# Kernel tuning notes

Hardware: AMD Instinct MI355X
Metric: run time of the kernel (lower is better)

Reference implementation:

```python
import jax, jax.numpy as jnp
import numpy as np

HEADS = 8
HIDDEN = 512
SEQ = 1024
BATCH = 8
SCALE = 1.2
TOPK = round(0.05 * SEQ)  # 51, as in mode='stocastic'


def setup_inputs() -> dict:
    key = jax.random.key(0)
    ks = jax.random.split(key, 12)
    d = HIDDEN
    s = 0.02
    return {
        "Query_x": jax.random.normal(ks[0], (BATCH, SEQ, d), jnp.float32),
        "KeyandValue_x": jax.random.normal(ks[1], (BATCH, SEQ, d), jnp.float32),
        "Wq": jax.random.normal(ks[2], (d, d), jnp.float32) * s,
        "bq": jnp.zeros((d,), jnp.float32),
        "Wk": jax.random.normal(ks[3], (d, d), jnp.float32) * s,
        "bk": jnp.zeros((d,), jnp.float32),
        "Wv": jax.random.normal(ks[4], (d, d), jnp.float32) * s,
        "bv": jnp.zeros((d,), jnp.float32),
        "Wo": jax.random.normal(ks[5], (d, d), jnp.float32) * s,
        "bo": jnp.zeros((d,), jnp.float32),
        "randidx": jax.random.randint(ks[6], (round(0.1 * SEQ),), 0, SEQ, jnp.int32),
    }


def _split_heads(x, B, S):
    # torch: split last dim into heads chunks, cat along dim 0 -> [heads*B, S, dk]
    dk = HIDDEN // HEADS
    return x.reshape(B, S, HEADS, dk).transpose(2, 0, 1, 3).reshape(HEADS * B, S, dk)


def _merge_heads(x, B, S):
    dk = HIDDEN // HEADS
    return x.reshape(HEADS, B, S, dk).transpose(1, 2, 0, 3).reshape(B, S, HIDDEN)


def moderate_attention(a, randidx):
    # a: [N, S, L] softmaxed attention. Scale top-k + random columns by SCALE,
    # then renormalize rows. torch scatter_ writes a*SCALE gathered from the
    # pre-scatter tensor, so duplicate indices are idempotent -> boolean mask.
    N, S, L = a.shape
    _, idx = jax.lax.top_k(a, TOPK)                       # [N, S, k]
    rand_b = jnp.broadcast_to(randidx.astype(idx.dtype), (N, S, randidx.shape[0]))
    all_idx = jnp.concatenate([idx, rand_b], axis=-1)      # [N, S, k+r]
    n_ix = jnp.arange(N)[:, None, None]
    q_ix = jnp.arange(S)[None, :, None]
    sel = jnp.zeros(a.shape, bool).at[n_ix, q_ix, all_idx].set(True)
    a2 = jnp.where(sel, a * SCALE, a)
    return a2 / jnp.sum(a2, axis=-1, keepdims=True)


def reference(Query_x, KeyandValue_x, Wq, bq, Wk, bk, Wv, bv, Wo, bo, randidx):
    B, S, _ = Query_x.shape
    dk = HIDDEN // HEADS
    Q = _split_heads(Query_x @ Wq + bq, B, S)          # [H*B, S, dk]
    K = _split_heads(KeyandValue_x @ Wk + bk, B, S)
    V = _split_heads(KeyandValue_x @ Wv + bv, B, S)
    scores = jnp.einsum('nqd,nkd->nqk', Q, K) / jnp.sqrt(jnp.float32(dk))
    a = jax.nn.softmax(scores, axis=-1)
    a = moderate_attention(a, randidx)
    out = jnp.einsum('nqk,nkd->nqd', a, V)
    return _merge_heads(out, B, S) @ Wo + bo
```

## Files before the change

### kernel.cpp

```cpp
#include <hip/hip_runtime.h>
#include <stdint.h>

typedef unsigned short ushort_t;
typedef __bf16 bf16x8 __attribute__((ext_vector_type(8)));
typedef _Float16 f16x8v __attribute__((ext_vector_type(8)));
typedef __fp16 fp16x2 __attribute__((ext_vector_type(2)));
typedef float f32x4 __attribute__((ext_vector_type(4)));

#define SEQ   1024
#define DK    64
#define TOPK_N 51
#define RSCALE 1.2f
#define LOG2E    1.44269504089f
#define LOG2_12  0.26303440583f

#define OFF_WT  0
#define OFF_Q   (4*512*512)
#define OFF_K   (OFF_Q  + 64*1024*64)
#define OFF_V   (OFF_K  + 64*1024*64)
#define OFF_A   (OFF_V  + 64*1024*64)
#define OFF_MASK (OFF_A + 8192*512)

static __device__ __forceinline__ ushort_t f2bf(float f){
  union { float f; unsigned u; } x; x.f = f;
  unsigned r = x.u + 0x7FFFu + ((x.u >> 16) & 1u);
  return (ushort_t)(r >> 16);
}
static __device__ __forceinline__ ushort_t f2h(float f){
  union { _Float16 h; ushort_t u; } x; x.h = (_Float16)f; return x.u;
}
static __device__ __forceinline__ float h2f(ushort_t u){
  union { ushort_t u; _Float16 h; } x; x.u = u; return (float)x.h;
}
static __device__ __forceinline__ unsigned pk2(float a, float b){
  union { fp16x2 h; unsigned u; } x;
  x.h = __builtin_amdgcn_cvt_pkrtz(a, b);
  return x.u;
}
static __device__ __forceinline__ unsigned pkrne(float a, float b){
  return (unsigned)f2h(a) | ((unsigned)f2h(b) << 16);
}
static __device__ __forceinline__ bf16x8 frag16(const ushort_t* p){
  union { uint4 u; bf16x8 b; } x; x.u = *(const uint4*)p; return x.b;
}
static __device__ __forceinline__ f16x8v frag16h(const ushort_t* p){
  union { uint4 u; f16x8v h; } x; x.u = *(const uint4*)p; return x.h;
}
static __device__ __forceinline__ void gll16(const ushort_t* g, ushort_t* lds){
  __builtin_amdgcn_global_load_lds((const __attribute__((address_space(1))) unsigned*)g,
                                   (__attribute__((address_space(3))) unsigned*)lds,
                                   16, 0, 0);
}

__global__ __launch_bounds__(256) void prep_k(
    const float* Wq, const float* Wk, const float* Wv, const float* Wo,
    const int* ridx, int nrand, ushort_t* ws){
  __shared__ ushort_t t[64][72];
  __shared__ unsigned wds[64];
  int bid = blockIdx.x, tid = threadIdx.x;

  if (bid < 256){
    int rb = bid;
    int z = rb >> 6, rem = rb & 63;
    const float* W = z==0?Wq: z==1?Wk: z==2?Wv: Wo;
    ushort_t* O = ws + OFF_WT + (size_t)z*512*512;
    int kt = (rem >> 3)*64, nt = (rem & 7)*64;
    int r0 = tid>>3, c8 = (tid&7)*8;
    #pragma unroll
    for (int p=0;p<2;p++){
      int r = p*32 + r0;
      float4 a = *(const float4*)&W[(size_t)(kt+r)*512 + nt + c8];
      float4 b = *(const float4*)&W[(size_t)(kt+r)*512 + nt + c8 + 4];
      t[r][c8+0]=f2bf(a.x); t[r][c8+1]=f2bf(a.y); t[r][c8+2]=f2bf(a.z); t[r][c8+3]=f2bf(a.w);
      t[r][c8+4]=f2bf(b.x); t[r][c8+5]=f2bf(b.y); t[r][c8+6]=f2bf(b.z); t[r][c8+7]=f2bf(b.w);
    }
    __syncthreads();
    #pragma unroll
    for (int p=0;p<2;p++){
      int r = p*32 + r0;
      union { ushort_t s[8]; uint4 u; } tmp;
      #pragma unroll
      for (int j=0;j<8;j++) tmp.s[j] = t[c8+j][r];
      *(uint4*)&O[(size_t)(nt+r)*512 + kt + c8] = tmp.u;
    }
  } else {
    if (tid < 64) wds[tid] = 0;
    __syncthreads();
    for (int i = tid; i < nrand; i += 256){
      int col = ridx[i];
      atomicOr(&wds[(col >> 3) & 63], 1u << (((col >> 9) << 3) | (col & 7)));
    }
    __syncthreads();
    if (tid < 64) (ws + OFF_MASK)[tid] = (ushort_t)wds[tid];
  }
}

__global__ __launch_bounds__(256, 3) void gemm_k(ushort_t* ws,
    const float* qx, const float* kvx,
    const float* bq, const float* bk, const float* bv, const float* bo,
    float* dout, int base_mode){
  int mode = base_mode + blockIdx.z;
  const float*    Xf = (mode==0)? qx : kvx;
  const ushort_t* Xb = ws + OFF_A;
  const ushort_t* WT = ws + OFF_WT + (size_t)mode*(512*512);
  const float* bias  = (mode==0)?bq:(mode==1)?bk:(mode==2)?bv:bo;
  ushort_t* out = (mode==0)? ws+OFF_Q : (mode==1)? ws+OFF_K : ws+OFF_V;

  __shared__ ushort_t sA[3][128*32];
  __shared__ ushort_t sB[3][128*32];
  int tid = threadIdx.x, lane = tid & 63, w = tid >> 6;
  int wm = w & 1, wn = w >> 1;
  int m0 = blockIdx.y * 128, n0 = blockIdx.x * 128;
  int r16 = lane & 15, quad = lane >> 4;
  int srow = tid >> 2, sch = tid & 3;
  int arow = tid >> 1, acp = (tid & 1) * 2;

  const f32x4 zero = {0.f,0.f,0.f,0.f};
  f32x4 acc[4][4];
  #pragma unroll
  for (int i=0;i<4;i++)
    #pragma unroll
    for (int j=0;j<4;j++) acc[i][j] = zero;

  #define STAGE_B(t, buf)                                                      \
    {                                                                          \
      int k0 = (t)*32;                                                         \
      _Pragma("unroll")                                                        \
      for (int p=0;p<2;p++){                                                   \
        int row = p*64 + srow;                                                 \
        int gch = sch ^ ((row >> 1) & 3);                                      \
        gll16(WT + (size_t)(n0+row)*512 + k0 + gch*8, &sB[buf][(p*64 + (w<<4))*32]); \
      }                                                                        \
    }
  #define STAGE_A3(t, buf)                                                     \
    {                                                                          \
      int k0 = (t)*32;                                                         \
      _Pragma("unroll")                                                        \
      for (int p=0;p<2;p++){                                                   \
        int row = p*64 + srow;                                                 \
        int gch = sch ^ ((row >> 1) & 3);                                      \
        gll16(Xb + (size_t)(m0+row)*512 + k0 + gch*8, &sA[buf][(p*64 + (w<<4))*32]); \
      }                                                                        \
    }
  #define AISSUE(t, rg)                                                        \
    {                                                                          \
      int k0 = (t)*32;                                                         \
      _Pragma("unroll")                                                        \
      for (int c=0;c<2;c++){                                                   \
        int lc = (acp + c) ^ ((arow >> 1) & 3);                                \
        const float* sp = Xf + (size_t)(m0+arow)*512 + k0 + lc*8;              \
        rg[c*2+0] = *(const float4*)sp;                                        \
        rg[c*2+1] = *(const float4*)(sp + 4);                                  \
      }                                                                        \
    }
  #define AWRITE(buf, rg)                                                      \
    {                                                                          \
      _Pragma("unroll")                                                        \
      for (int c=0;c<2;c++){                                                   \
        union { ushort_t s[8]; uint4 u; } pkk;                                 \
        pkk.s[0]=f2bf(rg[c*2+0].x); pkk.s[1]=f2bf(rg[c*2+0].y);                \
        pkk.s[2]=f2bf(rg[c*2+0].z); pkk.s[3]=f2bf(rg[c*2+0].w);                \
        pkk.s[4]=f2bf(rg[c*2+1].x); pkk.s[5]=f2bf(rg[c*2+1].y);                \
        pkk.s[6]=f2bf(rg[c*2+1].z); pkk.s[7]=f2bf(rg[c*2+1].w);                \
        *(uint4*)&sA[buf][arow*32 + (acp + c)*8] = pkk.u;                      \
      }                                                                        \
    }

  if (base_mode == 3){
    STAGE_A3(0, 0); STAGE_B(0, 0);
    STAGE_A3(1, 1); STAGE_B(1, 1);
    #pragma unroll
    for (int t = 0; t < 16; t++){
      if (t < 15) asm volatile("s_waitcnt vmcnt(4)" ::: "memory");
      else        asm volatile("s_waitcnt vmcnt(0)" ::: "memory");
      __builtin_amdgcn_s_barrier();
      asm volatile("" ::: "memory");
      if (t < 14){ STAGE_A3(t+2, (t+2)%3); STAGE_B(t+2, (t+2)%3); }
      int buf = t % 3;
      bf16x8 aF[4], bF[4];
      #pragma unroll
      for (int i=0;i<4;i++){
        int row = wm*64 + i*16 + r16;
        aF[i] = frag16(&sA[buf][row*32 + ((quad ^ ((row >> 1) & 3))*8)]);
      }
      #pragma unroll
      for (int j=0;j<4;j++){
        int row = wn*64 + j*16 + r16;
        bF[j] = frag16(&sB[buf][row*32 + ((quad ^ ((row >> 1) & 3))*8)]);
      }
      __builtin_amdgcn_s_setprio(1);
      #pragma unroll
      for (int i=0;i<4;i++)
        #pragma unroll
        for (int j=0;j<4;j++)
          acc[i][j] = __builtin_amdgcn_mfma_f32_16x16x32_bf16(aF[i], bF[j], acc[i][j], 0,0,0);
      __builtin_amdgcn_s_setprio(0);
    }
  } else {
    float4 rg[4];
    AISSUE(0, rg); STAGE_B(0, 0);
    for (int t = 0; t < 16; t++){
      float4 rn[4];
      if (t < 15){
        AISSUE(t+1, rn);
        STAGE_B(t+1, (t+1)%3);
        asm volatile("s_waitcnt vmcnt(6)" ::: "memory");
      } else {
        asm volatile("s_waitcnt vmcnt(0)" ::: "memory");
      }
      int abuf = t & 1;
      AWRITE(abuf, rg);
      asm volatile("s_waitcnt lgkmcnt(0)" ::: "memory");
      __builtin_amdgcn_s_barrier();
      asm volatile("" ::: "memory");
      int bbuf = t % 3;
      bf16x8 aF[4], bF[4];
      #pragma unroll
      for (int i=0;i<4;i++){
        int row = wm*64 + i*16 + r16;
        aF[i] = frag16(&sA[abuf][row*32 + ((quad ^ ((row >> 1) & 3))*8)]);
      }
      #pragma unroll
      for (int j=0;j<4;j++){
        int row = wn*64 + j*16 + r16;
        bF[j] = frag16(&sB[bbuf][row*32 + ((quad ^ ((row >> 1) & 3))*8)]);
      }
      __builtin_amdgcn_s_setprio(1);
      #pragma unroll
      for (int i=0;i<4;i++)
        #pragma unroll
        for (int j=0;j<4;j++)
          acc[i][j] = __builtin_amdgcn_mfma_f32_16x16x32_bf16(aF[i], bF[j], acc[i][j], 0,0,0);
      __builtin_amdgcn_s_setprio(0);
      #pragma unroll
      for (int c=0;c<4;c++) rg[c] = rn[c];
    }
  }
  #undef STAGE_B
  #undef STAGE_A3
  #undef AISSUE
  #undef AWRITE

  #pragma unroll
  for (int i=0;i<4;i++){
    int rowbase = m0 + wm*64 + i*16 + quad*4;
    #pragma unroll
    for (int j=0;j<4;j++){
      int col = n0 + wn*64 + j*16 + r16;
      float bsv = bias[col];
      if (mode == 3){
        #pragma unroll
        for (int r=0;r<4;r++)
          dout[(size_t)(rowbase+r)*512 + col] = acc[i][j][r] + bsv;
      } else if (mode == 2){
        int b = rowbase >> 10, s = rowbase & 1023;
        int h = col >> 6, d = col & 63;
        int nh = h*8 + b;
        union { ushort_t sh[4]; uint2 u2; } pk;
        #pragma unroll
        for (int r=0;r<4;r++) pk.sh[r] = f2h(acc[i][j][r] + bsv);
        *(uint2*)&out[ (((size_t)nh*128 + (s>>3))*64 + d)*8 + (s&4) ] = pk.u2;
      } else if (mode == 1){
        int b = rowbase >> 10;
        int h = col >> 6, d = col & 63;
        int nh = h*8 + b;
        size_t base = (size_t)nh*65536 + (size_t)(d>>3)*8192 + (d&7);
        #pragma unroll
        for (int r=0;r<4;r++){
          int s = (rowbase + r) & 1023;
          out[ base + (size_t)s*8 ] = f2bf(acc[i][j][r] + bsv);
        }
      } else {
        int h = col >> 6, d = col & 63;
        #pragma unroll
        for (int r=0;r<4;r++){
          int row = rowbase + r;
          int b = row >> 10, s = row & 1023;
          int nh = h*8 + b;
          out[ ((size_t)nh*1024 + s)*64 + d ] = f2bf((acc[i][j][r] + bsv)*0.125f);
        }
      }
    }
  }
}

__global__ __launch_bounds__(256, 4) void attn_k(const ushort_t* ws_q, const ushort_t* ws_k,
     const ushort_t* ws_v, const ushort_t* maskp, ushort_t* attn){
  __shared__ __align__(16) ushort_t sS[16*1024];

  int tid = threadIdx.x, lane = tid&63, w = tid>>6;
  int r16 = lane&15, quad = lane>>4;
  int gid = blockIdx.x;
  int n  = (gid & 7)*8 + ((gid >> 3) >> 6);
  int q0 = ((gid >> 3) & 63) * 16;
  const ushort_t* Qn = ws_q + (size_t)n*SEQ*DK;
  const ushort_t* Kn = ws_k + (size_t)n*SEQ*DK;
  const ushort_t* Vb = ws_v + (size_t)n*SEQ*DK;

  unsigned rmask = (unsigned)maskp[lane];

  bf16x8 aQ[2];
  #pragma unroll
  for (int t=0;t<2;t++)
    aQ[t] = frag16(Qn + (size_t)(q0 + r16)*64 + t*32 + quad*8);

  const f32x4 zero = {0.f,0.f,0.f,0.f};

  #pragma unroll
  for (int half=0; half<2; half++){
    f32x4 acc[8];
    #pragma unroll
    for (int i=0;i<8;i++) acc[i] = zero;
    #pragma unroll
    for (int grp=0; grp<2; grp++){
      int c = half*2 + grp;
      bf16x8 bF[8];
      #pragma unroll
      for (int u=0;u<4;u++){
        int key = c*256 + w*64 + u*16 + r16;
        bF[u*2+0] = frag16(Kn + ((size_t)(quad    )*1024 + key)*8);
        bF[u*2+1] = frag16(Kn + ((size_t)(4 + quad)*1024 + key)*8);
      }
      __builtin_amdgcn_s_setprio(1);
      #pragma unroll
      for (int u=0;u<4;u++){
        int t8 = grp*4 + u;
        acc[t8] = __builtin_amdgcn_mfma_f32_16x16x32_bf16(bF[u*2+0], aQ[0], acc[t8], 0,0,0);
        acc[t8] = __builtin_amdgcn_mfma_f32_16x16x32_bf16(bF[u*2+1], aQ[1], acc[t8], 0,0,0);
      }
      __builtin_amdgcn_s_setprio(0);
    }
    int rs = r16 & 7;
    #pragma unroll
    for (int grp=0; grp<2; grp++)
      #pragma unroll
      for (int u=0;u<4;u++){
        int kb = (half*2+grp)*256 + w*64 + u*16 + quad*4;
        f32x4 a = acc[grp*4+u];
        uint2 o;
        o.x = pkrne(a[0], a[1]);
        o.y = pkrne(a[2], a[3]);
        *(uint2*)(sS + r16*1024 + (((kb>>3) ^ rs) << 3) + (kb & 4)) = o;
      }
  }
  __syncthreads();

  float v[4][16];
  float vmax[4];
  #pragma unroll
  for (int r=0;r<4;r++){
    int row = w*4 + r, rs = row & 7;
    const ushort_t* bp = sS + row*1024 + ((lane ^ rs) * 8);
    uint4 lo4 = *(const uint4*)bp;
    uint4 hi4 = *(const uint4*)(bp + 512);
    unsigned wl[8] = {lo4.x, lo4.y, lo4.z, lo4.w, hi4.x, hi4.y, hi4.z, hi4.w};
    float m = -3.0e38f;
    #pragma unroll
    for (int k=0;k<8;k++){
      float a = h2f((ushort_t)(wl[k] & 0xffffu));
      float b = h2f((ushort_t)(wl[k] >> 16));
      v[r][2*k] = a; v[r][2*k+1] = b;
      m = fmaxf(m, fmaxf(a, b));
    }
    vmax[r] = m;
  }
  #pragma unroll
  for (int r=0;r<4;r++)
    #pragma unroll
    for (int j=0;j<16;j++)
      asm volatile("" : "+v"(v[r][j]));

  #pragma unroll
  for (int off=32; off>=1; off>>=1)
    #pragma unroll
    for (int r=0;r<4;r++) vmax[r] = fmaxf(vmax[r], __shfl_xor(vmax[r], off));

  float blo[4], bhi[4];
  #pragma unroll
  for (int r=0;r<4;r++){ bhi[r] = vmax[r]; blo[r] = vmax[r] - 1.0f; }
  #pragma unroll 1
  for (int it=0; it<9; it++){
    #pragma unroll
    for (int r=0;r<4;r++){
      float mid = 0.5f*(blo[r]+bhi[r]);
      int cnt = 0;
      #pragma unroll
      for (int j=0;j<16;j++)
        cnt += __popcll(__ballot(v[r][j] >= mid));
      bool ge = (cnt >= TOPK_N);
      blo[r] = ge ? mid : blo[r];
      bhi[r] = ge ? bhi[r] : mid;
    }
  }
  float fb[16];
  #pragma unroll
  for (int j=0;j<16;j++) fb[j] = ((rmask >> j) & 1u) ? LOG2_12 : 0.0f;
  float sC = LOG2_12;
  asm volatile("" : "+v"(sC));

  float ls[4];
  #pragma unroll
  for (int r=0;r<4;r++){
    float thr = blo[r], s = 0.f;
    #pragma unroll
    for (int j=0;j<16;j++){
      float tb = (v[r][j] >= thr) ? sC : fb[j];
      float e = __builtin_amdgcn_exp2f(
                  __builtin_fmaf(v[r][j] - vmax[r], LOG2E, tb));
      v[r][j] = e; s += e;
    }
    ls[r] = s;
  }
  #pragma unroll
  for (int off=32; off>=1; off>>=1)
    #pragma unroll
    for (int r=0;r<4;r++) ls[r] += __shfl_xor(ls[r], off);
  #pragma unroll
  for (int r=0;r<4;r++){
    int row = w*4 + r, rs = row & 7;
    float rinv = 1.0f / ls[r];
    ushort_t* bp = sS + row*1024 + ((lane ^ rs) * 8);
    uint4 o0, o1;
    o0.x = pk2(v[r][0]*rinv,  v[r][1]*rinv);
    o0.y = pk2(v[r][2]*rinv,  v[r][3]*rinv);
    o0.z = pk2(v[r][4]*rinv,  v[r][5]*rinv);
    o0.w = pk2(v[r][6]*rinv,  v[r][7]*rinv);
    o1.x = pk2(v[r][8]*rinv,  v[r][9]*rinv);
    o1.y = pk2(v[r][10]*rinv, v[r][11]*rinv);
    o1.z = pk2(v[r][12]*rinv, v[r][13]*rinv);
    o1.w = pk2(v[r][14]*rinv, v[r][15]*rinv);
    *(uint4*)bp = o0;
    *(uint4*)(bp + 512) = o1;
  }
  __syncthreads();

  f32x4 oa0 = zero, oa1 = zero;
  int dd = w*16 + r16;
  #pragma unroll
  for (int kb2=0; kb2<8; kb2++){
    f16x8v bV[4], aP[4];
    #pragma unroll
    for (int u=0;u<4;u++){
      int g8 = (kb2*4 + u)*4 + quad;
      bV[u] = frag16h(Vb + ((size_t)g8*64 + dd)*8);
      aP[u] = frag16h(sS + r16*1024 + ((g8 ^ (r16&7))*8));
    }
    __builtin_amdgcn_s_setprio(1);
    #pragma unroll
    for (int u=0;u<4;u++){
      if (u&1) oa1 = __builtin_amdgcn_mfma_f32_16x16x32_f16(aP[u], bV[u], oa1, 0,0,0);
      else     oa0 = __builtin_amdgcn_mfma_f32_16x16x32_f16(aP[u], bV[u], oa0, 0,0,0);
    }
    __builtin_amdgcn_s_setprio(0);
  }
  f32x4 oacc = oa0 + oa1;

  int h = n >> 3, b = n & 7;
  #pragma unroll
  for (int r=0;r<4;r++){
    int s = q0 + quad*4 + r;
    attn[ ((size_t)(b*1024 + s))*512 + h*64 + w*16 + r16 ] = f2bf(oacc[r]);
  }
}

extern "C" void kernel_launch(void* const* d_in, const int* in_sizes, int n_in,
                              void* d_out, int out_size, void* d_ws, size_t ws_size,
                              hipStream_t stream){
  const float* Qx  = (const float*)d_in[0];
  const float* KVx = (const float*)d_in[1];
  const float* Wq  = (const float*)d_in[2];
  const float* bq  = (const float*)d_in[3];
  const float* Wk  = (const float*)d_in[4];
  const float* bk  = (const float*)d_in[5];
  const float* Wv  = (const float*)d_in[6];
  const float* bv  = (const float*)d_in[7];
  const float* Wo  = (const float*)d_in[8];
  const float* bo  = (const float*)d_in[9];
  const int* ridx  = (const int*)d_in[10];
  int nrand = in_sizes[10];
  ushort_t* ws = (ushort_t*)d_ws;
  float* dout = (float*)d_out;

  prep_k<<<257, 256, 0, stream>>>(Wq, Wk, Wv, Wo, ridx, nrand, ws);
  gemm_k<<<dim3(4,64,3), 256, 0, stream>>>(ws, Qx, KVx, bq, bk, bv, bo, dout, 0);
  attn_k<<<4096, 256, 0, stream>>>(ws+OFF_Q, ws+OFF_K, ws+OFF_V, ws+OFF_MASK, ws+OFF_A);
  gemm_k<<<dim3(4,64,1), 256, 0, stream>>>(ws, Qx, KVx, bq, bk, bv, bo, dout, 3);
}
```

Before: 221.1 us.

## Fuse K and V projections to share the converted activation tile

The QKV projection kernel now launches two z-slices instead of three. The KV slice loads and converts the fp32 KeyandValue activation tile to bf16 once and multiplies it against both Wk and Wv, keeping two accumulator sets. This halves the reads and conversions of the KV input. In exchange, KV blocks do twice the MFMA work, use more registers and shared memory (launch bounds drop to 2), and the grid becomes load-imbalanced between Q blocks and KV blocks. The output projection is split into its own specialized kernel.

```diff
diff --git a/kernel.cpp b/kernel.cpp
--- a/kernel.cpp
+++ b/kernel.cpp
@@ -95,19 +95,17 @@
   }
 }
 
-__global__ __launch_bounds__(256, 3) void gemm_k(ushort_t* ws,
+__global__ __launch_bounds__(256, 2) void gemmqkv_k(ushort_t* ws,
     const float* qx, const float* kvx,
-    const float* bq, const float* bk, const float* bv, const float* bo,
-    float* dout, int base_mode){
-  int mode = base_mode + blockIdx.z;
-  const float*    Xf = (mode==0)? qx : kvx;
-  const ushort_t* Xb = ws + OFF_A;
-  const ushort_t* WT = ws + OFF_WT + (size_t)mode*(512*512);
-  const float* bias  = (mode==0)?bq:(mode==1)?bk:(mode==2)?bv:bo;
-  ushort_t* out = (mode==0)? ws+OFF_Q : (mode==1)? ws+OFF_K : ws+OFF_V;
-
-  __shared__ ushort_t sA[3][128*32];
-  __shared__ ushort_t sB[3][128*32];
+    const float* bq, const float* bk, const float* bv){
+  bool isKV = (blockIdx.z != 0);
+  const float* Xf = isKV ? kvx : qx;
+  const ushort_t* WT0 = ws + OFF_WT + (size_t)(isKV ? 1 : 0)*512*512;
+  const ushort_t* WT1 = ws + OFF_WT + (size_t)2*512*512;
+
+  __shared__ ushort_t sA [2][128*32];
+  __shared__ ushort_t sB0[3][128*32];
+  __shared__ ushort_t sB1[3][128*32];
   int tid = threadIdx.x, lane = tid & 63, w = tid >> 6;
   int wm = w & 1, wn = w >> 1;
   int m0 = blockIdx.y * 128, n0 = blockIdx.x * 128;
@@ -116,30 +114,20 @@
   int arow = tid >> 1, acp = (tid & 1) * 2;
 
   const f32x4 zero = {0.f,0.f,0.f,0.f};
-  f32x4 acc[4][4];
+  f32x4 acc0[4][4], acc1[4][4];
   #pragma unroll
   for (int i=0;i<4;i++)
     #pragma unroll
-    for (int j=0;j<4;j++) acc[i][j] = zero;
-
-  #define STAGE_B(t, buf)                                                      \
+    for (int j=0;j<4;j++){ acc0[i][j] = zero; acc1[i][j] = zero; }
+
+  #define STAGE_B(WT, t, buf, SB)                                              \
     {                                                                          \
       int k0 = (t)*32;                                                         \
       _Pragma("unroll")                                                        \
       for (int p=0;p<2;p++){                                                   \
         int row = p*64 + srow;                                                 \
         int gch = sch ^ ((row >> 1) & 3);                                      \
-        gll16(WT + (size_t)(n0+row)*512 + k0 + gch*8, &sB[buf][(p*64 + (w<<4))*32]); \
-      }                                                                        \
-    }
-  #define STAGE_A3(t, buf)                                                     \
-    {                                                                          \
-      int k0 = (t)*32;                                                         \
-      _Pragma("unroll")                                                        \
-      for (int p=0;p<2;p++){                                                   \
-        int row = p*64 + srow;                                                 \
-        int gch = sch ^ ((row >> 1) & 3);                                      \
-        gll16(Xb + (size_t)(m0+row)*512 + k0 + gch*8, &sA[buf][(p*64 + (w<<4))*32]); \
+        gll16(WT + (size_t)(n0+row)*512 + k0 + gch*8, &SB[buf][(p*64 + (w<<4))*32]); \
       }                                                                        \
     }
   #define AISSUE(t, rg)                                                        \
@@ -166,78 +154,66 @@
       }                                                                        \
     }
 
-  if (base_mode == 3){
-    STAGE_A3(0, 0); STAGE_B(0, 0);
-    STAGE_A3(1, 1); STAGE_B(1, 1);
-    #pragma unroll
-    for (int t = 0; t < 16; t++){
-      if (t < 15) asm volatile("s_waitcnt vmcnt(4)" ::: "memory");
-      else        asm volatile("s_waitcnt vmcnt(0)" ::: "memory");
-      __builtin_amdgcn_s_barrier();
-      asm volatile("" ::: "memory");
-      if (t < 14){ STAGE_A3(t+2, (t+2)%3); STAGE_B(t+2, (t+2)%3); }
-      int buf = t % 3;
-      bf16x8 aF[4], bF[4];
-      #pragma unroll
-      for (int i=0;i<4;i++){
-        int row = wm*64 + i*16 + r16;
-        aF[i] = frag16(&sA[buf][row*32 + ((quad ^ ((row >> 1) & 3))*8)]);
+  float4 rg[4];
+  AISSUE(0, rg);
+  STAGE_B(WT0, 0, 0, sB0);
+  if (isKV) STAGE_B(WT1, 0, 0, sB1);
+
+  for (int t = 0; t < 16; t++){
+    float4 rn[4];
+    if (t < 15){
+      AISSUE(t+1, rn);
+      STAGE_B(WT0, t+1, (t+1)%3, sB0);
+      if (isKV){
+        STAGE_B(WT1, t+1, (t+1)%3, sB1);
+        asm volatile("s_waitcnt vmcnt(8)" ::: "memory");
+      } else {
+        asm volatile("s_waitcnt vmcnt(6)" ::: "memory");
       }
+    } else {
+      asm volatile("s_waitcnt vmcnt(0)" ::: "memory");
+    }
+    int abuf = t & 1, bbuf = t % 3;
+    AWRITE(abuf, rg);
+    asm volatile("s_waitcnt lgkmcnt(0)" ::: "memory");
+    __builtin_amdgcn_s_barrier();
+    asm volatile("" ::: "memory");
+    bf16x8 aF[4], bF[4];
+    #pragma unroll
+    for (int i=0;i<4;i++){
+      int row = wm*64 + i*16 + r16;
+      aF[i] = frag16(&sA[abuf][row*32 + ((quad ^ ((row >> 1) & 3))*8)]);
+    }
+    #pragma unroll
+    for (int j=0;j<4;j++){
+      int row = wn*64 + j*16 + r16;
+      bF[j] = frag16(&sB0[bbuf][row*32 + ((quad ^ ((row >> 1) & 3))*8)]);
+    }
+    __builtin_amdgcn_s_setprio(1);
+    #pragma unroll
+    for (int i=0;i<4;i++)
+      #pragma unroll
+      for (int j=0;j<4;j++)
+        acc0[i][j] = __builtin_amdgcn_mfma_f32_16x16x32_bf16(aF[i], bF[j], acc0[i][j], 0,0,0);
+    __builtin_amdgcn_s_setprio(0);
+    if (isKV){
       #pragma unroll
       for (int j=0;j<4;j++){
         int row = wn*64 + j*16 + r16;
-        bF[j] = frag16(&sB[buf][row*32 + ((quad ^ ((row >> 1) & 3))*8)]);
+        bF[j] = frag16(&sB1[bbuf][row*32 + ((quad ^ ((row >> 1) & 3))*8)]);
       }
       __builtin_amdgcn_s_setprio(1);
       #pragma unroll
       for (int i=0;i<4;i++)
         #pragma unroll
         for (int j=0;j<4;j++)
-          acc[i][j] = __builtin_amdgcn_mfma_f32_16x16x32_bf16(aF[i], bF[j], acc[i][j], 0,0,0);
+          acc1[i][j] = __builtin_amdgcn_mfma_f32_16x16x32_bf16(aF[i], bF[j], acc1[i][j], 0,0,0);
       __builtin_amdgcn_s_setprio(0);
     }
-  } else {
-    float4 rg[4];
-    AISSUE(0, rg); STAGE_B(0, 0);
-    for (int t = 0; t < 16; t++){
-      float4 rn[4];
-      if (t < 15){
-        AISSUE(t+1, rn);
-        STAGE_B(t+1, (t+1)%3);
-        asm volatile("s_waitcnt vmcnt(6)" ::: "memory");
-      } else {
-        asm volatile("s_waitcnt vmcnt(0)" ::: "memory");
-      }
-      int abuf = t & 1;
-      AWRITE(abuf, rg);
-      asm volatile("s_waitcnt lgkmcnt(0)" ::: "memory");
-      __builtin_amdgcn_s_barrier();
-      asm volatile("" ::: "memory");
-      int bbuf = t % 3;
-      bf16x8 aF[4], bF[4];
-      #pragma unroll
-      for (int i=0;i<4;i++){
-        int row = wm*64 + i*16 + r16;
-        aF[i] = frag16(&sA[abuf][row*32 + ((quad ^ ((row >> 1) & 3))*8)]);
-      }
-      #pragma unroll
-      for (int j=0;j<4;j++){
-        int row = wn*64 + j*16 + r16;
-        bF[j] = frag16(&sB[bbuf][row*32 + ((quad ^ ((row >> 1) & 3))*8)]);
-      }
-      __builtin_amdgcn_s_setprio(1);
-      #pragma unroll
-      for (int i=0;i<4;i++)
-        #pragma unroll
-        for (int j=0;j<4;j++)
-          acc[i][j] = __builtin_amdgcn_mfma_f32_16x16x32_bf16(aF[i], bF[j], acc[i][j], 0,0,0);
-      __builtin_amdgcn_s_setprio(0);
-      #pragma unroll
-      for (int c=0;c<4;c++) rg[c] = rn[c];
-    }
+    #pragma unroll
+    for (int c=0;c<4;c++) rg[c] = rn[c];
   }
   #undef STAGE_B
-  #undef STAGE_A3
   #undef AISSUE
   #undef AWRITE
 
@@ -247,39 +223,118 @@
     #pragma unroll
     for (int j=0;j<4;j++){
       int col = n0 + wn*64 + j*16 + r16;
-      float bsv = bias[col];
-      if (mode == 3){
-        #pragma unroll
-        for (int r=0;r<4;r++)
-          dout[(size_t)(rowbase+r)*512 + col] = acc[i][j][r] + bsv;
-      } else if (mode == 2){
-        int b = rowbase >> 10, s = rowbase & 1023;
-        int h = col >> 6, d = col & 63;
-        int nh = h*8 + b;
-        union { ushort_t sh[4]; uint2 u2; } pk;
-        #pragma unroll
-        for (int r=0;r<4;r++) pk.sh[r] = f2h(acc[i][j][r] + bsv);
-        *(uint2*)&out[ (((size_t)nh*128 + (s>>3))*64 + d)*8 + (s&4) ] = pk.u2;
-      } else if (mode == 1){
-        int b = rowbase >> 10;
-        int h = col >> 6, d = col & 63;
-        int nh = h*8 + b;
-        size_t base = (size_t)nh*65536 + (size_t)(d>>3)*8192 + (d&7);
-        #pragma unroll
-        for (int r=0;r<4;r++){
-          int s = (rowbase + r) & 1023;
-          out[ base + (size_t)s*8 ] = f2bf(acc[i][j][r] + bsv);
-        }
-      } else {
-        int h = col >> 6, d = col & 63;
+      int h = col >> 6, d = col & 63;
+      if (!isKV){
+        float bsv = bq[col];
+        ushort_t* out = ws + OFF_Q;
         #pragma unroll
         for (int r=0;r<4;r++){
           int row = rowbase + r;
           int b = row >> 10, s = row & 1023;
           int nh = h*8 + b;
-          out[ ((size_t)nh*1024 + s)*64 + d ] = f2bf((acc[i][j][r] + bsv)*0.125f);
+          out[ ((size_t)nh*1024 + s)*64 + d ] = f2bf((acc0[i][j][r] + bsv)*0.125f);
+        }
+      } else {
+        {
+          float bsv = bk[col];
+          ushort_t* out = ws + OFF_K;
+          int b = rowbase >> 10;
+          int nh = h*8 + b;
+          size_t base = (size_t)nh*65536 + (size_t)(d>>3)*8192 + (d&7);
+          #pragma unroll
+          for (int r=0;r<4;r++){
+            int s = (rowbase + r) & 1023;
+            out[ base + (size_t)s*8 ] = f2bf(acc0[i][j][r] + bsv);
+          }
+        }
+        {
+          float bsv = bv[col];
+          ushort_t* out = ws + OFF_V;
+          int b = rowbase >> 10, s = rowbase & 1023;
+          int nh = h*8 + b;
+          union { ushort_t sh[4]; uint2 u2; } pk;
+          #pragma unroll
+          for (int r=0;r<4;r++) pk.sh[r] = f2h(acc1[i][j][r] + bsv);
+          *(uint2*)&out[ (((size_t)nh*128 + (s>>3))*64 + d)*8 + (s&4) ] = pk.u2;
         }
       }
+    }
+  }
+}
+
+__global__ __launch_bounds__(256, 3) void gemm3_k(ushort_t* ws,
+    const float* bo, float* dout){
+  const ushort_t* Xb = ws + OFF_A;
+  const ushort_t* WT = ws + OFF_WT + (size_t)3*(512*512);
+
+  __shared__ ushort_t sA[3][128*32];
+  __shared__ ushort_t sB[3][128*32];
+  int tid = threadIdx.x, lane = tid & 63, w = tid >> 6;
+  int wm = w & 1, wn = w >> 1;
+  int m0 = blockIdx.y * 128, n0 = blockIdx.x * 128;
+  int r16 = lane & 15, quad = lane >> 4;
+  int srow = tid >> 2, sch = tid & 3;
+
+  const f32x4 zero = {0.f,0.f,0.f,0.f};
+  f32x4 acc[4][4];
+  #pragma unroll
+  for (int i=0;i<4;i++)
+    #pragma unroll
+    for (int j=0;j<4;j++) acc[i][j] = zero;
+
+  #define STAGE(t, buf)                                                        \
+    {                                                                          \
+      int k0 = (t)*32;                                                         \
+      _Pragma("unroll")                                                        \
+      for (int p=0;p<2;p++){                                                   \
+        int row = p*64 + srow;                                                 \
+        int gch = sch ^ ((row >> 1) & 3);                                      \
+        gll16(Xb + (size_t)(m0+row)*512 + k0 + gch*8, &sA[buf][(p*64 + (w<<4))*32]); \
+        gll16(WT + (size_t)(n0+row)*512 + k0 + gch*8, &sB[buf][(p*64 + (w<<4))*32]); \
+      }                                                                        \
+    }
+
+  STAGE(0, 0);
+  STAGE(1, 1);
+  #pragma unroll
+  for (int t = 0; t < 16; t++){
+    if (t < 15) asm volatile("s_waitcnt vmcnt(4)" ::: "memory");
+    else        asm volatile("s_waitcnt vmcnt(0)" ::: "memory");
+    __builtin_amdgcn_s_barrier();
+    asm volatile("" ::: "memory");
+    if (t < 14) STAGE(t+2, (t+2)%3);
+    int buf = t % 3;
+    bf16x8 aF[4], bF[4];
+    #pragma unroll
+    for (int i=0;i<4;i++){
+      int row = wm*64 + i*16 + r16;
+      aF[i] = frag16(&sA[buf][row*32 + ((quad ^ ((row >> 1) & 3))*8)]);
+    }
+    #pragma unroll
+    for (int j=0;j<4;j++){
+      int row = wn*64 + j*16 + r16;
+      bF[j] = frag16(&sB[buf][row*32 + ((quad ^ ((row >> 1) & 3))*8)]);
+    }
+    __builtin_amdgcn_s_setprio(1);
+    #pragma unroll
+    for (int i=0;i<4;i++)
+      #pragma unroll
+      for (int j=0;j<4;j++)
+        acc[i][j] = __builtin_amdgcn_mfma_f32_16x16x32_bf16(aF[i], bF[j], acc[i][j], 0,0,0);
+    __builtin_amdgcn_s_setprio(0);
+  }
+  #undef STAGE
+
+  #pragma unroll
+  for (int i=0;i<4;i++){
+    int rowbase = m0 + wm*64 + i*16 + quad*4;
+    #pragma unroll
+    for (int j=0;j<4;j++){
+      int col = n0 + wn*64 + j*16 + r16;
+      float bsv = bo[col];
+      #pragma unroll
+      for (int r=0;r<4;r++)
+        dout[(size_t)(rowbase+r)*512 + col] = acc[i][j][r] + bsv;
     }
   }
 }
@@ -482,7 +537,7 @@
   float* dout = (float*)d_out;
 
   prep_k<<<257, 256, 0, stream>>>(Wq, Wk, Wv, Wo, ridx, nrand, ws);
-  gemm_k<<<dim3(4,64,3), 256, 0, stream>>>(ws, Qx, KVx, bq, bk, bv, bo, dout, 0);
+  gemmqkv_k<<<dim3(4,64,2), 256, 0, stream>>>(ws, Qx, KVx, bq, bk, bv);
   attn_k<<<4096, 256, 0, stream>>>(ws+OFF_Q, ws+OFF_K, ws+OFF_V, ws+OFF_MASK, ws+OFF_A);
-  gemm_k<<<dim3(4,64,1), 256, 0, stream>>>(ws, Qx, KVx, bq, bk, bv, bo, dout, 3);
-}
+  gemm3_k<<<dim3(4,64,1), 256, 0, stream>>>(ws, bo, dout);
+}
```

Result: faster. 215.1 us (-2.7%).
